# Optimization experiments

Hardware: AMD Instinct MI355X
Metric: run time of the kernel (lower is better)

## Reference

```python
import jax, jax.numpy as jnp
import numpy as np

N = 131072          # number of feature vectors
F_DIM = 512         # feature_dim
D = 256             # latent_dim
K = 2048            # num_embeddings
BETA = 0.25         # commitment_cost


def _mlp(x, params):
    # params: list of (W, b); ReLU after every layer (matches nn.Sequential)
    for W, b in params:
        x = jax.nn.relu(x @ W + b)
    return x


def setup_inputs() -> dict:
    key = jax.random.key(0)
    ks = jax.random.split(key, 14)

    def lin(k, fan_in, fan_out):
        bound = 1.0 / np.sqrt(fan_in)
        kw, kb = jax.random.split(k)
        W = jax.random.uniform(kw, (fan_in, fan_out), jnp.float32, -bound, bound)
        b = jax.random.uniform(kb, (fan_out,), jnp.float32, -bound, bound)
        return W, b

    enc_w1, enc_b1 = lin(ks[1], F_DIM, 64)
    enc_w2, enc_b2 = lin(ks[2], 64, 128)
    enc_w3, enc_b3 = lin(ks[3], 128, D)
    dec_w1, dec_b1 = lin(ks[4], D, 128)
    dec_w2, dec_b2 = lin(ks[5], 128, 64)
    dec_w3, dec_b3 = lin(ks[6], 64, F_DIM)
    emb = jax.random.uniform(ks[7], (K, D), jnp.float32, -1.0 / K, 1.0 / K)
    x = jax.random.normal(ks[0], (N, F_DIM), jnp.float32)
    return {
        "x": x,
        "enc_w1": enc_w1, "enc_b1": enc_b1,
        "enc_w2": enc_w2, "enc_b2": enc_b2,
        "enc_w3": enc_w3, "enc_b3": enc_b3,
        "dec_w1": dec_w1, "dec_b1": dec_b1,
        "dec_w2": dec_w2, "dec_b2": dec_b2,
        "dec_w3": dec_w3, "dec_b3": dec_b3,
        "emb": emb,
    }


def reference(x, enc_w1, enc_b1, enc_w2, enc_b2, enc_w3, enc_b3,
              dec_w1, dec_b1, dec_w2, dec_b2, dec_w3, dec_b3, emb):
    enc = [(enc_w1, enc_b1), (enc_w2, enc_b2), (enc_w3, enc_b3)]
    dec = [(dec_w1, dec_b1), (dec_w2, dec_b2), (dec_w3, dec_b3)]

    z_e = _mlp(x, enc)  # (N, D)

    # ||z - e||^2 = ||z||^2 - 2 z.e + ||e||^2   (avoids (N,K,D) broadcast)
    z_sq = jnp.sum(z_e * z_e, axis=-1, keepdims=True)      # (N, 1)
    e_sq = jnp.sum(emb * emb, axis=-1)                      # (K,)
    distances = z_sq - 2.0 * (z_e @ emb.T) + e_sq           # (N, K)
    idx = jnp.argmin(distances, axis=1)                     # (N,)
    z_q = emb[idx]                                          # (N, D)

    commitment_loss = BETA * jnp.mean((jax.lax.stop_gradient(z_q) - z_e) ** 2)
    embedding_loss = jnp.mean((z_q - jax.lax.stop_gradient(z_e)) ** 2)
    quantization_loss = embedding_loss + commitment_loss

    # straight-through estimator
    z_q_st = z_e + jax.lax.stop_gradient(z_q - z_e)

    x_recon = _mlp(z_q_st, dec)
    recon_loss = jnp.mean((x_recon - x) ** 2)
    loss = recon_loss + quantization_loss

    z_latent = jax.lax.stop_gradient(z_q_st)
    return (z_latent, loss)
```

## Files before the change

kernel.cpp:

```cpp
#include <hip/hip_runtime.h>

#define NROWS 131072
#define KE 2048
#define CAND_CAP 8192

typedef unsigned long long u64_t;
typedef unsigned int u32;
typedef __attribute__((ext_vector_type(8))) short bf16x8;
typedef __attribute__((ext_vector_type(4))) float f32x4;

__device__ __forceinline__ unsigned f32_key(float f) {
  unsigned u = __float_as_uint(f);
  return (u & 0x80000000u) ? ~u : (u | 0x80000000u);
}

__device__ __forceinline__ unsigned short bf16_rne(float f) {
  unsigned u = __float_as_uint(f);
  u += 0x7FFFu + ((u >> 16) & 1u);
  return (unsigned short)(u >> 16);
}

template <int MODE>
__global__ __launch_bounds__(256) void gemm64(
    const float* __restrict__ A, const float* __restrict__ B,
    const float* __restrict__ bias, float* __restrict__ C,
    int M, int N, int K,
    const int* __restrict__ gidx) {
  __shared__ __align__(16) float As[16][68];
  __shared__ __align__(16) float Bs[16][68];

  const int tid = threadIdx.x;
  const int tx = tid & 15;
  const int ty = tid >> 4;
  const int arow = blockIdx.x * 64;
  const int bcol = blockIdx.y * 64;

  const int lr = tid >> 2;
  const int lc = (tid & 3) * 4;
  int ga = arow + lr;
  if (MODE == 1) ga = gidx[ga];
  const float* Ap = A + (size_t)ga * K + lc;

  const int bkr = tid >> 4;
  const int bc4 = (tid & 15) * 4;
  const float* Bp = B + (size_t)bkr * N + bcol + bc4;

  float acc[4][4] = {};

  for (int kt = 0; kt < K; kt += 16) {
    float4 av = *reinterpret_cast<const float4*>(Ap);
    As[lc + 0][lr] = av.x;
    As[lc + 1][lr] = av.y;
    As[lc + 2][lr] = av.z;
    As[lc + 3][lr] = av.w;
    float4 bv = *reinterpret_cast<const float4*>(Bp);
    *reinterpret_cast<float4*>(&Bs[bkr][bc4]) = bv;
    Bp += (size_t)16 * N;
    Ap += 16;
    __syncthreads();
#pragma unroll
    for (int k = 0; k < 16; ++k) {
      float4 a = *reinterpret_cast<const float4*>(&As[k][ty * 4]);
      float4 b = *reinterpret_cast<const float4*>(&Bs[k][tx * 4]);
      acc[0][0] += a.x * b.x; acc[0][1] += a.x * b.y; acc[0][2] += a.x * b.z; acc[0][3] += a.x * b.w;
      acc[1][0] += a.y * b.x; acc[1][1] += a.y * b.y; acc[1][2] += a.y * b.z; acc[1][3] += a.y * b.w;
      acc[2][0] += a.z * b.x; acc[2][1] += a.z * b.y; acc[2][2] += a.z * b.z; acc[2][3] += a.z * b.w;
      acc[3][0] += a.w * b.x; acc[3][1] += a.w * b.y; acc[3][2] += a.w * b.z; acc[3][3] += a.w * b.w;
    }
    __syncthreads();
  }

#pragma unroll
  for (int i = 0; i < 4; ++i) {
    const int row = arow + ty * 4 + i;
    float4 v;
    v.x = fmaxf(acc[i][0] + bias[bcol + tx * 4 + 0], 0.f);
    v.y = fmaxf(acc[i][1] + bias[bcol + tx * 4 + 1], 0.f);
    v.z = fmaxf(acc[i][2] + bias[bcol + tx * 4 + 2], 0.f);
    v.w = fmaxf(acc[i][3] + bias[bcol + tx * 4 + 3], 0.f);
    *reinterpret_cast<float4*>(&C[(size_t)row * N + bcol + tx * 4]) = v;
  }
}

template <int MODE>
__global__ __launch_bounds__(256) void gemm128(
    const float* __restrict__ A, const float* __restrict__ B,
    const float* __restrict__ bias, float* __restrict__ C,
    int N, int K,
    const int* __restrict__ gidx,
    const float* __restrict__ X,
    float* __restrict__ parts) {
  __shared__ __align__(16) char smem[17408];
  float (*As)[132] = (float(*)[132])smem;
  float (*Bs)[132] = (float(*)[132])(smem + 8448);

  const int tid = threadIdx.x;
  const int tx = tid & 15;
  const int ty = tid >> 4;
  const int arow = blockIdx.x * 128;
  const int bcol = blockIdx.y * 128;

  const int r0 = tid >> 2;
  const int r1 = r0 + 64;
  const int lc = (tid & 3) * 4;
  int ga0 = arow + r0, ga1 = arow + r1;
  if (MODE == 1) { ga0 = gidx[ga0]; ga1 = gidx[ga1]; }
  const float* Ap0 = A + (size_t)ga0 * K + lc;
  const float* Ap1 = A + (size_t)ga1 * K + lc;

  const int bk0 = tid >> 5;
  const int bc0 = (tid & 31) * 4;
  const float* Bp0 = B + (size_t)bk0 * N + bcol + bc0;
  const float* Bp1 = B + (size_t)(bk0 + 8) * N + bcol + bc0;

  float acc[8][8] = {};

  for (int kt = 0; kt < K; kt += 16) {
    float4 a0 = *reinterpret_cast<const float4*>(Ap0);
    float4 a1 = *reinterpret_cast<const float4*>(Ap1);
    As[lc + 0][r0] = a0.x; As[lc + 1][r0] = a0.y; As[lc + 2][r0] = a0.z; As[lc + 3][r0] = a0.w;
    As[lc + 0][r1] = a1.x; As[lc + 1][r1] = a1.y; As[lc + 2][r1] = a1.z; As[lc + 3][r1] = a1.w;
    float4 b0 = *reinterpret_cast<const float4*>(Bp0);
    float4 b1 = *reinterpret_cast<const float4*>(Bp1);
    *reinterpret_cast<float4*>(&Bs[bk0][bc0]) = b0;
    *reinterpret_cast<float4*>(&Bs[bk0 + 8][bc0]) = b1;
    Bp0 += (size_t)16 * N; Bp1 += (size_t)16 * N;
    Ap0 += 16; Ap1 += 16;
    __syncthreads();
#pragma unroll
    for (int k = 0; k < 16; ++k) {
      float4 av0 = *reinterpret_cast<const float4*>(&As[k][ty * 4]);
      float4 av1 = *reinterpret_cast<const float4*>(&As[k][64 + ty * 4]);
      float4 bv0 = *reinterpret_cast<const float4*>(&Bs[k][tx * 4]);
      float4 bv1 = *reinterpret_cast<const float4*>(&Bs[k][64 + tx * 4]);
      const float a[8] = {av0.x, av0.y, av0.z, av0.w, av1.x, av1.y, av1.z, av1.w};
      const float b[8] = {bv0.x, bv0.y, bv0.z, bv0.w, bv1.x, bv1.y, bv1.z, bv1.w};
#pragma unroll
      for (int i = 0; i < 8; ++i)
#pragma unroll
        for (int j = 0; j < 8; ++j) acc[i][j] += a[i] * b[j];
    }
    __syncthreads();
  }

#pragma unroll
  for (int i = 0; i < 8; ++i) {
    const int row = arow + (i >> 2) * 64 + ty * 4 + (i & 3);
    const int c0 = bcol + tx * 4;
    const int c1 = bcol + 64 + tx * 4;
    float4 v0, v1;
    v0.x = fmaxf(acc[i][0] + bias[c0 + 0], 0.f);
    v0.y = fmaxf(acc[i][1] + bias[c0 + 1], 0.f);
    v0.z = fmaxf(acc[i][2] + bias[c0 + 2], 0.f);
    v0.w = fmaxf(acc[i][3] + bias[c0 + 3], 0.f);
    v1.x = fmaxf(acc[i][4] + bias[c1 + 0], 0.f);
    v1.y = fmaxf(acc[i][5] + bias[c1 + 1], 0.f);
    v1.z = fmaxf(acc[i][6] + bias[c1 + 2], 0.f);
    v1.w = fmaxf(acc[i][7] + bias[c1 + 3], 0.f);
    *reinterpret_cast<float4*>(&C[(size_t)row * N + c0]) = v0;
    *reinterpret_cast<float4*>(&C[(size_t)row * N + c1]) = v1;
  }
}

__global__ __launch_bounds__(256) void cvt_z16t(const float* __restrict__ z_e,
                                                unsigned short* __restrict__ z16t) {
  const int c = blockIdx.x * 256 + threadIdx.x;
  const int lane = c & 63;
  const int kb = (c >> 6) & 7;
  const int fr = (c >> 9) & 3;
  const int w = (c >> 11) & 3;
  const int rowblk = c >> 13;
  const int row = rowblk * 256 + w * 64 + fr * 16 + (lane & 15);
  const int k0 = kb * 32 + (lane >> 4) * 8;
  const float* p = z_e + (size_t)row * 256 + k0;
  const float4 v0 = *reinterpret_cast<const float4*>(p);
  const float4 v1 = *reinterpret_cast<const float4*>(p + 4);
  const float f[8] = {v0.x, v0.y, v0.z, v0.w, v1.x, v1.y, v1.z, v1.w};
  unsigned short s[8];
#pragma unroll
  for (int j = 0; j < 8; ++j) s[j] = bf16_rne(f[j]);
  uint4 o;
  o.x = (u32)s[0] | ((u32)s[1] << 16);
  o.y = (u32)s[2] | ((u32)s[3] << 16);
  o.z = (u32)s[4] | ((u32)s[5] << 16);
  o.w = (u32)s[6] | ((u32)s[7] << 16);
  *reinterpret_cast<uint4*>(z16t + (size_t)c * 8) = o;
}

__global__ __launch_bounds__(256) void cvt_e16f(const float* __restrict__ emb,
                                                unsigned short* __restrict__ e16f) {
  const int c = blockIdx.x * 256 + threadIdx.x;
  const int l = c & 63;
  const int fc = (c >> 6) & 7;
  const int t = c >> 9;
  const int kb = t & 7;
  const int ct = t >> 3;
  const int col = ct * 128 + fc * 16 + (l & 15);
  const int k0 = kb * 32 + (l >> 4) * 8;
  const float* p = emb + (size_t)col * 256 + k0;
  const float4 v0 = *reinterpret_cast<const float4*>(p);
  const float4 v1 = *reinterpret_cast<const float4*>(p + 4);
  const float f[8] = {v0.x, v0.y, v0.z, v0.w, v1.x, v1.y, v1.z, v1.w};
  unsigned short s8[8];
#pragma unroll
  for (int j = 0; j < 8; ++j) s8[j] = bf16_rne(f[j]);
  uint4 o;
  o.x = (u32)s8[0] | ((u32)s8[1] << 16);
  o.y = (u32)s8[2] | ((u32)s8[3] << 16);
  o.z = (u32)s8[4] | ((u32)s8[5] << 16);
  o.w = (u32)s8[6] | ((u32)s8[7] << 16);
  *reinterpret_cast<uint4*>(e16f + (size_t)c * 8) = o;
}

__global__ __launch_bounds__(256) void cvt_rows16(const float* __restrict__ src,
                                                  unsigned short* __restrict__ dst) {
  const int i = blockIdx.x * 256 + threadIdx.x;
  const float4 v0 = *reinterpret_cast<const float4*>(src + (size_t)i * 8);
  const float4 v1 = *reinterpret_cast<const float4*>(src + (size_t)i * 8 + 4);
  const float f[8] = {v0.x, v0.y, v0.z, v0.w, v1.x, v1.y, v1.z, v1.w};
  unsigned short s[8];
#pragma unroll
  for (int j = 0; j < 8; ++j) s[j] = bf16_rne(f[j]);
  uint4 o;
  o.x = (u32)s[0] | ((u32)s[1] << 16);
  o.y = (u32)s[2] | ((u32)s[3] << 16);
  o.z = (u32)s[4] | ((u32)s[5] << 16);
  o.w = (u32)s[6] | ((u32)s[7] << 16);
  *reinterpret_cast<uint4*>(dst + (size_t)i * 8) = o;
}

__global__ __launch_bounds__(256) void cvt_w16f(const float* __restrict__ W,
                                                unsigned short* __restrict__ Wf,
                                                int N, int total) {
  const int c = blockIdx.x * 256 + threadIdx.x;
  if (c >= total) return;
  const int l = c & 63;
  const int f = c >> 6;
  const int ng = N >> 4;
  const int cg = f % ng;
  const int kb = f / ng;
  const int col = cg * 16 + (l & 15);
  const int k0 = kb * 32 + ((l >> 4) & 3) * 8;
  unsigned short s[8];
#pragma unroll
  for (int j = 0; j < 8; ++j) s[j] = bf16_rne(W[(size_t)(k0 + j) * N + col]);
  uint4 o;
  o.x = (u32)s[0] | ((u32)s[1] << 16);
  o.y = (u32)s[2] | ((u32)s[3] << 16);
  o.z = (u32)s[4] | ((u32)s[5] << 16);
  o.w = (u32)s[6] | ((u32)s[7] << 16);
  *reinterpret_cast<uint4*>(Wf + (size_t)c * 8) = o;
}

__global__ __launch_bounds__(256, 1) void dist_g256(
    const unsigned short* __restrict__ z16t, const unsigned short* __restrict__ e16f,
    const float* __restrict__ zf, const float* __restrict__ ef,
    const float* __restrict__ zsq, const float* __restrict__ esq,
    const float* __restrict__ maxesq, u64_t* __restrict__ keys) {
  __shared__ float esq_lds[2048];
  __shared__ float me1_lds[256];
  __shared__ float rowmin_lds[256];
  __shared__ unsigned cand[CAND_CAP];
  __shared__ unsigned cnt;

  const int tid = threadIdx.x;
  const int l = tid & 63;
  const int w = tid >> 6;
  const int l15 = tid & 15;
  const int lk = (tid >> 4) & 3;
  const int arow = blockIdx.x * 256;

  if (tid == 0) cnt = 0;
  {
    for (int i = tid; i < 2048; i += 256) esq_lds[i] = esq[i];
    me1_lds[tid] = 0.009765625f * sqrtf(zsq[arow + tid]);
    rowmin_lds[tid] = 3.402823466e38f;
  }
  const float semax = sqrtf(maxesq[0]);

  bf16x8 a[4][8];
  {
    const char* zb = (const char*)z16t + (size_t)blockIdx.x * 131072 + w * 32768 + l * 16;
#pragma unroll
    for (int fr = 0; fr < 4; ++fr)
#pragma unroll
      for (int kb = 0; kb < 8; ++kb)
        a[fr][kb] = *reinterpret_cast<const bf16x8*>(zb + fr * 8192 + kb * 1024);
  }

  auto rescore = [&](unsigned e) {
    const int row = arow + (int)(e >> 11);
    const int col = (int)(e & 2047u);
    const float* zp = zf + (size_t)row * 256;
    const float* ep = ef + (size_t)col * 256;
    float p = 0.f;
#pragma unroll 8
    for (int k4 = 0; k4 < 256; k4 += 4) {
      const float4 zv = *reinterpret_cast<const float4*>(zp + k4);
      const float4 ev = *reinterpret_cast<const float4*>(ep + k4);
      p = fmaf(zv.x, ev.x, p);
      p = fmaf(zv.y, ev.y, p);
      p = fmaf(zv.z, ev.z, p);
      p = fmaf(zv.w, ev.w, p);
    }
    const float dsc = (zsq[row] - 2.f * p) + esq[col];
    const u64_t kk = ((u64_t)f32_key(dsc) << 32) | (unsigned)col;
    atomicMin(&keys[row], kk);
  };

  __syncthreads();

  const char* eb = (const char*)e16f + (size_t)l * 16;
  const int ct0 = (int)((blockIdx.x * 5u) & 15u);

  f32x4 acc[4][8];
#pragma unroll
  for (int fr = 0; fr < 4; ++fr)
#pragma unroll
    for (int fc = 0; fc < 8; ++fc) acc[fr][fc] = (f32x4){0.f, 0.f, 0.f, 0.f};

  bf16x8 bc[8], bn[8];
#pragma unroll
  for (int fc = 0; fc < 8; ++fc)
    bc[fc] = *reinterpret_cast<const bf16x8*>(eb + (size_t)(ct0 * 8) * 8192 + fc * 1024);

#pragma unroll 1
  for (int ctl = 0; ctl < 16; ++ctl) {
    const int ct = (ct0 + ctl) & 15;
#pragma unroll
    for (int kb = 0; kb < 8; ++kb) {
      const int nctl = (kb == 7) ? ctl + 1 : ctl;
      const int nkb = (kb == 7) ? 0 : kb + 1;
      if (nctl < 16) {
        const int nct = (ct0 + nctl) & 15;
        const char* tb = eb + (size_t)(nct * 8 + nkb) * 8192;
#pragma unroll
        for (int fc = 0; fc < 8; ++fc)
          bn[fc] = *reinterpret_cast<const bf16x8*>(tb + fc * 1024);
      }
#pragma unroll
      for (int fr = 0; fr < 4; ++fr)
#pragma unroll
        for (int fc = 0; fc < 8; ++fc)
          acc[fr][fc] = __builtin_amdgcn_mfma_f32_16x16x32_bf16(a[fr][kb], bc[fc], acc[fr][fc], 0, 0, 0);
#pragma unroll
      for (int fc = 0; fc < 8; ++fc) bc[fc] = bn[fc];
    }
    {
      float esqv[8], se[8];
#pragma unroll
      for (int fc = 0; fc < 8; ++fc) {
        esqv[fc] = esq_lds[ct * 128 + fc * 16 + l15];
        se[fc] = sqrtf(esqv[fc]);
      }
#pragma unroll
      for (int fr = 0; fr < 4; ++fr)
#pragma unroll
        for (int rg = 0; rg < 4; ++rg) {
          float s8[8];
          float lm = 3.402823466e38f;
#pragma unroll
          for (int fc = 0; fc < 8; ++fc) {
            s8[fc] = fmaf(-2.f, acc[fr][fc][rg], esqv[fc]);
            lm = fminf(lm, s8[fc]);
          }
#pragma unroll
          for (int m = 1; m < 16; m <<= 1) lm = fminf(lm, __shfl_xor(lm, m, 64));
          const int row = w * 64 + fr * 16 + lk * 4 + rg;
          const float rm = fminf(rowmin_lds[row], lm);
          if (l15 == 0) rowmin_lds[row] = rm;
          const float me1 = me1_lds[row];
#pragma unroll
          for (int fc = 0; fc < 8; ++fc) {
            const float thr = rm + me1 * (se[fc] + semax) + 1e-7f;
            if (s8[fc] <= thr) {
              const unsigned code =
                  ((unsigned)row << 11) | (unsigned)(ct * 128 + fc * 16 + l15);
              const unsigned idx = atomicAdd(&cnt, 1u);
              if (idx < CAND_CAP) cand[idx] = code;
              else rescore(code);
            }
          }
        }
#pragma unroll
      for (int fr = 0; fr < 4; ++fr)
#pragma unroll
        for (int fc = 0; fc < 8; ++fc) acc[fr][fc] = (f32x4){0.f, 0.f, 0.f, 0.f};
    }
  }

  __syncthreads();
  const unsigned nc = cnt < CAND_CAP ? cnt : CAND_CAP;
  for (unsigned i = tid; i < nc; i += 256) rescore(cand[i]);
}

template <int K, int NT, int NTOT, bool GATHER, bool LOSS>
__global__ __launch_bounds__(256, 1) void dec_mfma(
    const unsigned short* __restrict__ A16, const unsigned short* __restrict__ Wf,
    const float* __restrict__ bias, unsigned short* __restrict__ C16,
    const float* __restrict__ X, float* __restrict__ parts,
    const int* __restrict__ gidx) {
  constexpr int CH = K / 8;
  constexpr int KB = K / 32;
  constexpr int CG = NT / 16;
  constexpr int NB = NTOT / NT;
  __shared__ __align__(16) unsigned short Atile[128 * K];
  __shared__ int idx_l[128];
  __shared__ float rbuf[256];

  const int tid = threadIdx.x;
  const int l = tid & 63;
  const int w = tid >> 6;
  const int arow = (int)(blockIdx.x / NB) * 128;
  const int bcol = (int)(blockIdx.x % NB) * NT;

  if (GATHER) {
    if (tid < 128) idx_l[tid] = gidx[arow + tid];
    __syncthreads();
  }
  for (int q = tid; q < 128 * CH; q += 256) {
    const int r = q / CH;
    const int c = q % CH;
    const unsigned short* src = GATHER
        ? A16 + (size_t)idx_l[r] * K + c * 8
        : A16 + (size_t)(arow + r) * K + c * 8;
    const uint4 v = *reinterpret_cast<const uint4*>(src);
    *reinterpret_cast<uint4*>(&Atile[(r * CH + (c ^ (r & 7))) * 8]) = v;
  }

  bf16x8 wf[KB][CG];
#pragma unroll
  for (int kb = 0; kb < KB; ++kb)
#pragma unroll
    for (int cg = 0; cg < CG; ++cg)
      wf[kb][cg] = *reinterpret_cast<const bf16x8*>(
          Wf + ((size_t)(kb * (NTOT / 16) + bcol / 16 + cg) * 64 + l) * 8);

  __syncthreads();

  f32x4 acc[2][CG];
#pragma unroll
  for (int fr = 0; fr < 2; ++fr)
#pragma unroll
    for (int cg = 0; cg < CG; ++cg) acc[fr][cg] = (f32x4){0.f, 0.f, 0.f, 0.f};

#pragma unroll
  for (int kb = 0; kb < KB; ++kb) {
    bf16x8 af[2];
#pragma unroll
    for (int fr = 0; fr < 2; ++fr) {
      const int r = w * 32 + fr * 16 + (l & 15);
      const int c = (kb * 4 + ((l >> 4) & 3)) ^ (r & 7);
      af[fr] = *reinterpret_cast<const bf16x8*>(&Atile[(r * CH + c) * 8]);
    }
#pragma unroll
    for (int fr = 0; fr < 2; ++fr)
#pragma unroll
      for (int cg = 0; cg < CG; ++cg)
        acc[fr][cg] = __builtin_amdgcn_mfma_f32_16x16x32_bf16(af[fr], wf[kb][cg], acc[fr][cg], 0, 0, 0);
  }

  if (!LOSS) {
#pragma unroll
    for (int fr = 0; fr < 2; ++fr)
#pragma unroll
      for (int cg = 0; cg < CG; ++cg) {
        const int col = bcol + cg * 16 + (l & 15);
        const float bv = bias[col];
#pragma unroll
        for (int rg = 0; rg < 4; ++rg) {
          const int row = arow + w * 32 + fr * 16 + ((l >> 4) & 3) * 4 + rg;
          const float v = fmaxf(acc[fr][cg][rg] + bv, 0.f);
          C16[(size_t)row * NTOT + col] = bf16_rne(v);
        }
      }
  } else {
    float local = 0.f;
#pragma unroll
    for (int fr = 0; fr < 2; ++fr)
#pragma unroll
      for (int cg = 0; cg < CG; ++cg) {
        const int col = bcol + cg * 16 + (l & 15);
        const float bv = bias[col];
#pragma unroll
        for (int rg = 0; rg < 4; ++rg) {
          const int row = arow + w * 32 + fr * 16 + ((l >> 4) & 3) * 4 + rg;
          const float v = fmaxf(acc[fr][cg][rg] + bv, 0.f);
          const float d = v - X[(size_t)row * NTOT + col];
          local = fmaf(d, d, local);
        }
      }
    rbuf[tid] = local;
    __syncthreads();
    for (int off = 128; off > 0; off >>= 1) {
      if (tid < off) rbuf[tid] += rbuf[tid + off];
      __syncthreads();
    }
    if (tid == 0) parts[blockIdx.x] = rbuf[0];
  }
}

__global__ __launch_bounds__(256) void max_esq(const float* __restrict__ esq,
                                               float* __restrict__ outv) {
  __shared__ float red[256];
  float m = 0.f;
  for (int i = threadIdx.x; i < KE; i += 256) m = fmaxf(m, esq[i]);
  red[threadIdx.x] = m;
  __syncthreads();
  for (int off = 128; off > 0; off >>= 1) {
    if (threadIdx.x < off) red[threadIdx.x] = fmaxf(red[threadIdx.x], red[threadIdx.x + off]);
    __syncthreads();
  }
  if (threadIdx.x == 0) outv[0] = red[0];
}

__global__ __launch_bounds__(256) void rowsq(const float* __restrict__ src,
                                             float* __restrict__ dst, int rows) {
  const int sub = threadIdx.x >> 6;
  const int lane = threadIdx.x & 63;
  const int r = blockIdx.x * 4 + sub;
  if (r >= rows) return;
  const float* p = src + (size_t)r * 256;
  float s = 0.f;
#pragma unroll
  for (int j = 0; j < 4; ++j) {
    float v = p[lane + 64 * j];
    s += v * v;
  }
#pragma unroll
  for (int off = 32; off > 0; off >>= 1) s += __shfl_down(s, off, 64);
  if (lane == 0) dst[r] = s;
}

__global__ __launch_bounds__(256) void init_keys(u64_t* __restrict__ keys) {
  keys[(size_t)blockIdx.x * 256 + threadIdx.x] = ~0ull;
}

__global__ __launch_bounds__(256) void gather_quant(
    const u64_t* __restrict__ keys, const float* __restrict__ emb,
    const float* __restrict__ z_e, float* __restrict__ zlat,
    int* __restrict__ idx_out, float* __restrict__ qparts) {
  const int sub = threadIdx.x >> 6;
  const int lane = threadIdx.x & 63;
  const int r = blockIdx.x * 4 + sub;
  const int idx = (int)(keys[r] & 0xFFFFFFFFull);
  if (lane == 0) idx_out[r] = idx;
  float s = 0.f;
#pragma unroll
  for (int j = 0; j < 4; ++j) {
    const int d = lane + 64 * j;
    float e = emb[(size_t)idx * 256 + d];
    float z = z_e[(size_t)r * 256 + d];
    float df = e - z;
    s += df * df;
    zlat[(size_t)r * 256 + d] = z + df;
  }
#pragma unroll
  for (int off = 32; off > 0; off >>= 1) s += __shfl_down(s, off, 64);
  __shared__ float red[4];
  if (lane == 0) red[sub] = s;
  __syncthreads();
  if (threadIdx.x == 0) qparts[blockIdx.x] = (red[0] + red[1]) + (red[2] + red[3]);
}

__global__ __launch_bounds__(256) void final_loss(
    const float* __restrict__ qparts, int nq,
    const float* __restrict__ rparts, int nr, float* __restrict__ out) {
  const int tid = threadIdx.x;
  double sq = 0.0, sr = 0.0;
  for (int i = tid; i < nq; i += 256) sq += (double)qparts[i];
  for (int i = tid; i < nr; i += 256) sr += (double)rparts[i];
  __shared__ double bq[256], br[256];
  bq[tid] = sq;
  br[tid] = sr;
  __syncthreads();
  for (int off = 128; off > 0; off >>= 1) {
    if (tid < off) {
      bq[tid] += bq[tid + off];
      br[tid] += br[tid + off];
    }
    __syncthreads();
  }
  if (tid == 0) {
    double qm = bq[0] / ((double)NROWS * 256.0);
    double rm = br[0] / ((double)NROWS * 512.0);
    out[(size_t)NROWS * 256] = (float)(rm + 1.25 * qm);
  }
}

extern "C" void kernel_launch(void* const* d_in, const int* in_sizes, int n_in,
                              void* d_out, int out_size, void* d_ws, size_t ws_size,
                              hipStream_t stream) {
  const float* x   = (const float*)d_in[0];
  const float* ew1 = (const float*)d_in[1];
  const float* eb1 = (const float*)d_in[2];
  const float* ew2 = (const float*)d_in[3];
  const float* eb2 = (const float*)d_in[4];
  const float* ew3 = (const float*)d_in[5];
  const float* eb3 = (const float*)d_in[6];
  const float* dw1 = (const float*)d_in[7];
  const float* db1 = (const float*)d_in[8];
  const float* dw2 = (const float*)d_in[9];
  const float* db2 = (const float*)d_in[10];
  const float* dw3 = (const float*)d_in[11];
  const float* db3 = (const float*)d_in[12];
  const float* emb = (const float*)d_in[13];

  char* ws = (char*)d_ws;
  float* h1            = (float*)(ws);
  unsigned short* e16f = (unsigned short*)(ws);
  float* maxesq        = (float*)(ws + 2097152ull);
  unsigned short* emb16 = (unsigned short*)(ws + 4194304ull);
  unsigned short* w1f  = (unsigned short*)(ws + 5242880ull);
  unsigned short* w2f  = (unsigned short*)(ws + 5308416ull);
  unsigned short* w3f  = (unsigned short*)(ws + 5324800ull);
  float* h2            = (float*)(ws + 33554432ull);
  unsigned short* z16t = (unsigned short*)(ws + 33554432ull);
  unsigned short* h2_16 = (unsigned short*)(ws + 33554432ull);
  unsigned short* h1_16 = (unsigned short*)(ws + 67108864ull);
  float* z_e    = (float*)(ws + 100663296ull);
  float* zsq    = (float*)(ws + 234881024ull);
  float* esq    = (float*)(ws + 235405312ull);
  u64_t* keys   = (u64_t*)(ws + 235413504ull);
  int* idx      = (int*)(ws + 236462080ull);
  float* qparts = (float*)(ws + 236986368ull);
  float* rparts = (float*)(ws + 237117440ull);

  float* out = (float*)d_out;
  dim3 blk(256);

  gemm64<0><<<dim3(NROWS / 64, 1), blk, 0, stream>>>(x, ew1, eb1, h1, NROWS, 64, 512,
      nullptr);
  gemm128<0><<<dim3(NROWS / 128, 1), blk, 0, stream>>>(h1, ew2, eb2, h2,
      128, 64, nullptr, nullptr, nullptr);
  cvt_rows16<<<dim3(KE * 256 / 8 / 256), blk, 0, stream>>>(emb, emb16);
  cvt_w16f<<<dim3(16), blk, 0, stream>>>(dw1, w1f, 128, 4096);
  cvt_w16f<<<dim3(4), blk, 0, stream>>>(dw2, w2f, 64, 1024);
  cvt_w16f<<<dim3(16), blk, 0, stream>>>(dw3, w3f, 512, 4096);
  gemm128<0><<<dim3(NROWS / 128, 2), blk, 0, stream>>>(h2, ew3, eb3, z_e,
      256, 128, nullptr, nullptr, nullptr);

  rowsq<<<dim3(NROWS / 4), blk, 0, stream>>>(z_e, zsq, NROWS);
  rowsq<<<dim3(KE / 4), blk, 0, stream>>>(emb, esq, KE);
  max_esq<<<dim3(1), blk, 0, stream>>>(esq, maxesq);
  init_keys<<<dim3(NROWS / 256), blk, 0, stream>>>(keys);

  cvt_z16t<<<dim3(NROWS * 256 / 8 / 256), blk, 0, stream>>>(z_e, z16t);
  cvt_e16f<<<dim3(KE * 256 / 8 / 256), blk, 0, stream>>>(emb, e16f);

  dist_g256<<<dim3(NROWS / 256), blk, 0, stream>>>(z16t, e16f, z_e, emb, zsq, esq,
      maxesq, keys);

  gather_quant<<<dim3(NROWS / 4), blk, 0, stream>>>(keys, emb, z_e, out, idx, qparts);

  dec_mfma<256, 128, 128, true, false><<<dim3(NROWS / 128), blk, 0, stream>>>(
      emb16, w1f, db1, h2_16, nullptr, nullptr, idx);
  dec_mfma<128, 64, 64, false, false><<<dim3(NROWS / 128), blk, 0, stream>>>(
      h2_16, w2f, db2, h1_16, nullptr, nullptr, nullptr);
  dec_mfma<64, 256, 512, false, true><<<dim3((NROWS / 128) * 2), blk, 0, stream>>>(
      h1_16, w3f, db3, nullptr, x, rparts, nullptr);

  final_loss<<<dim3(1), blk, 0, stream>>>(qparts, NROWS / 4, rparts, 2048, out);
}
```

Measured before the change: 1.193 ms.

## Stage codebook tiles through LDS with async global-to-LDS double buffering

The distance kernel no longer has each wave load every codebook tile from global memory into registers. Tiles are now staged into a double-buffered LDS area with global_load_lds, so all four waves share one copy. The column loop is split into 32-column phases with fewer accumulators. This frees registers so two blocks can run per CU, and the row-min and threshold state moves from LDS into registers. The first column tile is scored twice: a first pass to seed the row minimum, then a pass that appends candidates. This adds a barrier every phase and halves the candidate buffer capacity, which can push more candidates onto the slow rescore path.

```diff
diff --git a/kernel.cpp b/kernel.cpp
--- a/kernel.cpp
+++ b/kernel.cpp
@@ -2,7 +2,7 @@
 
 #define NROWS 131072
 #define KE 2048
-#define CAND_CAP 8192
+#define CAND_CAP 4096
 
 typedef unsigned long long u64_t;
 typedef unsigned int u32;
@@ -18,6 +18,11 @@
   unsigned u = __float_as_uint(f);
   u += 0x7FFFu + ((u >> 16) & 1u);
   return (unsigned short)(u >> 16);
+}
+
+__device__ __forceinline__ void gl_lds16(const void* g, const void* l) {
+  __builtin_amdgcn_global_load_lds((const __attribute__((address_space(1))) u32*)g,
+                                   (__attribute__((address_space(3))) u32*)l, 16, 0, 0);
 }
 
 template <int MODE>
@@ -252,14 +257,13 @@
   *reinterpret_cast<uint4*>(Wf + (size_t)c * 8) = o;
 }
 
-__global__ __launch_bounds__(256, 1) void dist_g256(
+__global__ __launch_bounds__(256, 2) void dist_lds(
     const unsigned short* __restrict__ z16t, const unsigned short* __restrict__ e16f,
     const float* __restrict__ zf, const float* __restrict__ ef,
     const float* __restrict__ zsq, const float* __restrict__ esq,
     const float* __restrict__ maxesq, u64_t* __restrict__ keys) {
+  __shared__ __align__(16) unsigned short Bsm[2][8192];
   __shared__ float esq_lds[2048];
-  __shared__ float me1_lds[256];
-  __shared__ float rowmin_lds[256];
   __shared__ unsigned cand[CAND_CAP];
   __shared__ unsigned cnt;
 
@@ -271,11 +275,7 @@
   const int arow = blockIdx.x * 256;
 
   if (tid == 0) cnt = 0;
-  {
-    for (int i = tid; i < 2048; i += 256) esq_lds[i] = esq[i];
-    me1_lds[tid] = 0.009765625f * sqrtf(zsq[arow + tid]);
-    rowmin_lds[tid] = 3.402823466e38f;
-  }
+  for (int i = tid; i < 2048; i += 256) esq_lds[i] = esq[i];
   const float semax = sqrtf(maxesq[0]);
 
   bf16x8 a[4][8];
@@ -287,6 +287,17 @@
       for (int kb = 0; kb < 8; ++kb)
         a[fr][kb] = *reinterpret_cast<const bf16x8*>(zb + fr * 8192 + kb * 1024);
   }
+
+  float me1[4][4], runmin[4][4], rowmin[4][4];
+#pragma unroll
+  for (int fr = 0; fr < 4; ++fr)
+#pragma unroll
+    for (int rg = 0; rg < 4; ++rg) {
+      const int row = w * 64 + fr * 16 + lk * 4 + rg;
+      me1[fr][rg] = 0.009765625f * sqrtf(zsq[arow + row]);
+      runmin[fr][rg] = 3.402823466e38f;
+      rowmin[fr][rg] = 3.402823466e38f;
+    }
 
   auto rescore = [&](unsigned e) {
     const int row = arow + (int)(e >> 11);
@@ -308,90 +319,125 @@
     atomicMin(&keys[row], kk);
   };
 
+  const int ct0 = (int)((blockIdx.x * 5u) & 15u);
+  const char* ebase = (const char*)e16f + (size_t)l * 16;
+
+  auto phase_ctq = [&](int pp, int& ct, int& q) {
+    if (pp < 4) { ct = ct0; q = pp; }
+    else { ct = (ct0 + ((pp - 4) >> 2)) & 15; q = (pp - 4) & 3; }
+  };
+
+  auto stage = [&](int pp, int bsel) {
+    int ct, q;
+    phase_ctq(pp, ct, q);
+    char* dbase = (char*)&Bsm[bsel][0];
+#pragma unroll
+    for (int q2 = 0; q2 < 2; ++q2) {
+      const int kb = w * 2 + q2;
+#pragma unroll
+      for (int j = 0; j < 2; ++j) {
+        const int fc = q * 2 + j;
+        gl_lds16(ebase + ((size_t)((ct * 8 + kb) * 8 + fc) << 10),
+                 dbase + kb * 2048 + j * 1024);
+      }
+    }
+  };
+
+  f32x4 acc[4][2];
+#pragma unroll
+  for (int fr = 0; fr < 4; ++fr) {
+    acc[fr][0] = (f32x4){0.f, 0.f, 0.f, 0.f};
+    acc[fr][1] = (f32x4){0.f, 0.f, 0.f, 0.f};
+  }
+
+  stage(0, 0);
   __syncthreads();
 
-  const char* eb = (const char*)e16f + (size_t)l * 16;
-  const int ct0 = (int)((blockIdx.x * 5u) & 15u);
-
-  f32x4 acc[4][8];
-#pragma unroll
-  for (int fr = 0; fr < 4; ++fr)
-#pragma unroll
-    for (int fc = 0; fc < 8; ++fc) acc[fr][fc] = (f32x4){0.f, 0.f, 0.f, 0.f};
-
-  bf16x8 bc[8], bn[8];
-#pragma unroll
-  for (int fc = 0; fc < 8; ++fc)
-    bc[fc] = *reinterpret_cast<const bf16x8*>(eb + (size_t)(ct0 * 8) * 8192 + fc * 1024);
-
 #pragma unroll 1
-  for (int ctl = 0; ctl < 16; ++ctl) {
-    const int ct = (ct0 + ctl) & 15;
-#pragma unroll
-    for (int kb = 0; kb < 8; ++kb) {
-      const int nctl = (kb == 7) ? ctl + 1 : ctl;
-      const int nkb = (kb == 7) ? 0 : kb + 1;
-      if (nctl < 16) {
-        const int nct = (ct0 + nctl) & 15;
-        const char* tb = eb + (size_t)(nct * 8 + nkb) * 8192;
-#pragma unroll
-        for (int fc = 0; fc < 8; ++fc)
-          bn[fc] = *reinterpret_cast<const bf16x8*>(tb + fc * 1024);
+  for (int pp = 0; pp < 68; ++pp) {
+    const int bsel = pp & 1;
+    if (pp < 67) stage(pp + 1, bsel ^ 1);
+    {
+      const char* bp = (const char*)&Bsm[bsel][0];
+#pragma unroll
+      for (int kb = 0; kb < 8; ++kb) {
+        const bf16x8 b0 = *reinterpret_cast<const bf16x8*>(bp + kb * 2048 + l * 16);
+        const bf16x8 b1 = *reinterpret_cast<const bf16x8*>(bp + kb * 2048 + 1024 + l * 16);
+#pragma unroll
+        for (int fr = 0; fr < 4; ++fr) {
+          acc[fr][0] = __builtin_amdgcn_mfma_f32_16x16x32_bf16(a[fr][kb], b0, acc[fr][0], 0, 0, 0);
+          acc[fr][1] = __builtin_amdgcn_mfma_f32_16x16x32_bf16(a[fr][kb], b1, acc[fr][1], 0, 0, 0);
+        }
       }
+    }
+    {
+      int ct, q;
+      phase_ctq(pp, ct, q);
+      const int colbase = ct * 128 + q * 32;
+      const float ev0 = esq_lds[colbase + l15];
+      const float ev1 = esq_lds[colbase + 16 + l15];
+      const float m0 = sqrtf(ev0) + semax;
+      const float m1 = sqrtf(ev1) + semax;
+      const bool append = (pp >= 4);
 #pragma unroll
       for (int fr = 0; fr < 4; ++fr)
 #pragma unroll
-        for (int fc = 0; fc < 8; ++fc)
-          acc[fr][fc] = __builtin_amdgcn_mfma_f32_16x16x32_bf16(a[fr][kb], bc[fc], acc[fr][fc], 0, 0, 0);
-#pragma unroll
-      for (int fc = 0; fc < 8; ++fc) bc[fc] = bn[fc];
-    }
-    {
-      float esqv[8], se[8];
-#pragma unroll
-      for (int fc = 0; fc < 8; ++fc) {
-        esqv[fc] = esq_lds[ct * 128 + fc * 16 + l15];
-        se[fc] = sqrtf(esqv[fc]);
-      }
-#pragma unroll
-      for (int fr = 0; fr < 4; ++fr)
-#pragma unroll
         for (int rg = 0; rg < 4; ++rg) {
-          float s8[8];
-          float lm = 3.402823466e38f;
-#pragma unroll
-          for (int fc = 0; fc < 8; ++fc) {
-            s8[fc] = fmaf(-2.f, acc[fr][fc][rg], esqv[fc]);
-            lm = fminf(lm, s8[fc]);
-          }
-#pragma unroll
-          for (int m = 1; m < 16; m <<= 1) lm = fminf(lm, __shfl_xor(lm, m, 64));
-          const int row = w * 64 + fr * 16 + lk * 4 + rg;
-          const float rm = fminf(rowmin_lds[row], lm);
-          if (l15 == 0) rowmin_lds[row] = rm;
-          const float me1 = me1_lds[row];
-#pragma unroll
-          for (int fc = 0; fc < 8; ++fc) {
-            const float thr = rm + me1 * (se[fc] + semax) + 1e-7f;
-            if (s8[fc] <= thr) {
-              const unsigned code =
-                  ((unsigned)row << 11) | (unsigned)(ct * 128 + fc * 16 + l15);
+          const float s0 = fmaf(-2.f, acc[fr][0][rg], ev0);
+          const float s1 = fmaf(-2.f, acc[fr][1][rg], ev1);
+          runmin[fr][rg] = fminf(runmin[fr][rg], fminf(s0, s1));
+          if (append) {
+            const int row = w * 64 + fr * 16 + lk * 4 + rg;
+            const float rm = rowmin[fr][rg];
+            const float sc = me1[fr][rg];
+            if (s0 <= fmaf(sc, m0, rm) + 1e-7f) {
               const unsigned idx = atomicAdd(&cnt, 1u);
+              const unsigned code = ((unsigned)row << 11) | (unsigned)(colbase + l15);
+              if (idx < CAND_CAP) cand[idx] = code;
+              else rescore(code);
+            }
+            if (s1 <= fmaf(sc, m1, rm) + 1e-7f) {
+              const unsigned idx = atomicAdd(&cnt, 1u);
+              const unsigned code = ((unsigned)row << 11) | (unsigned)(colbase + 16 + l15);
               if (idx < CAND_CAP) cand[idx] = code;
               else rescore(code);
             }
           }
+          acc[fr][0][rg] = 0.f;
+          acc[fr][1][rg] = 0.f;
         }
-#pragma unroll
-      for (int fr = 0; fr < 4; ++fr)
-#pragma unroll
-        for (int fc = 0; fc < 8; ++fc) acc[fr][fc] = (f32x4){0.f, 0.f, 0.f, 0.f};
-    }
+      if (q == 3) {
+#pragma unroll
+        for (int fr = 0; fr < 4; ++fr)
+#pragma unroll
+          for (int rg = 0; rg < 4; ++rg) {
+            float lm = runmin[fr][rg];
+#pragma unroll
+            for (int m = 1; m < 16; m <<= 1) lm = fminf(lm, __shfl_xor(lm, m, 64));
+            rowmin[fr][rg] = lm;
+          }
+      }
+    }
+    __syncthreads();
   }
 
   __syncthreads();
   const unsigned nc = cnt < CAND_CAP ? cnt : CAND_CAP;
   for (unsigned i = tid; i < nc; i += 256) rescore(cand[i]);
+}
+
+__global__ __launch_bounds__(256) void max_esq(const float* __restrict__ esq,
+                                               float* __restrict__ outv) {
+  __shared__ float red[256];
+  float m = 0.f;
+  for (int i = threadIdx.x; i < KE; i += 256) m = fmaxf(m, esq[i]);
+  red[threadIdx.x] = m;
+  __syncthreads();
+  for (int off = 128; off > 0; off >>= 1) {
+    if (threadIdx.x < off) red[threadIdx.x] = fmaxf(red[threadIdx.x], red[threadIdx.x + off]);
+    __syncthreads();
+  }
+  if (threadIdx.x == 0) outv[0] = red[0];
 }
 
 template <int K, int NT, int NTOT, bool GATHER, bool LOSS>
@@ -498,20 +544,6 @@
     }
     if (tid == 0) parts[blockIdx.x] = rbuf[0];
   }
-}
-
-__global__ __launch_bounds__(256) void max_esq(const float* __restrict__ esq,
-                                               float* __restrict__ outv) {
-  __shared__ float red[256];
-  float m = 0.f;
-  for (int i = threadIdx.x; i < KE; i += 256) m = fmaxf(m, esq[i]);
-  red[threadIdx.x] = m;
-  __syncthreads();
-  for (int off = 128; off > 0; off >>= 1) {
-    if (threadIdx.x < off) red[threadIdx.x] = fmaxf(red[threadIdx.x], red[threadIdx.x + off]);
-    __syncthreads();
-  }
-  if (threadIdx.x == 0) outv[0] = red[0];
 }
 
 __global__ __launch_bounds__(256) void rowsq(const float* __restrict__ src,
@@ -648,7 +680,7 @@
   cvt_z16t<<<dim3(NROWS * 256 / 8 / 256), blk, 0, stream>>>(z_e, z16t);
   cvt_e16f<<<dim3(KE * 256 / 8 / 256), blk, 0, stream>>>(emb, e16f);
 
-  dist_g256<<<dim3(NROWS / 256), blk, 0, stream>>>(z16t, e16f, z_e, emb, zsq, esq,
+  dist_lds<<<dim3(NROWS / 256), blk, 0, stream>>>(z16t, e16f, z_e, emb, zsq, esq,
       maxesq, keys);
 
   gather_quant<<<dim3(NROWS / 4), blk, 0, stream>>>(keys, emb, z_e, out, idx, qparts);
```

Result: slower. 1.251 ms (+4.9%).
